# Kernel optimization log

Measured on AMD Instinct MI355X. Metric: run time of the kernel, lower is better.

## Reference

```python
import jax, jax.numpy as jnp
import numpy as np

B, Ci, H, W_ = 8, 64, 128, 128
C = 2 * Ci  # output channels of the 1x1 conv


def setup_inputs() -> dict:
    key = jax.random.key(0)
    kx, kw, kb = jax.random.split(key, 3)
    x = jax.random.normal(kx, (B, Ci, H, W_), dtype=jnp.float32)
    # Conv2d(Ci, 2*Ci, 1x1) parameters (kaiming-ish scale)
    Wc = jax.random.normal(kw, (C, Ci), dtype=jnp.float32) * (1.0 / np.float32(np.sqrt(Ci)))
    bc = jax.random.normal(kb, (C,), dtype=jnp.float32) * 0.01
    return {"x": x, "Wc": Wc, "bc": bc}


def _local_attention(y):
    # y: [B, C, H, W] conv output. 3x3 neighborhood self-attention, zero padding.
    b, c, h, w = y.shape
    yp = jnp.pad(y, ((0, 0), (0, 0), (1, 1), (1, 1)))
    # patches[:, :, k] = shifted neighborhood k (row-major 3x3, matching F.unfold order)
    patches = jnp.stack(
        [yp[:, :, di:di + h, dj:dj + w] for di in range(3) for dj in range(3)],
        axis=2,
    )  # [B, C, 9, H, W]
    mid = patches[:, :, 4]  # center pixel query, [B, C, H, W]
    scale = np.float32(1.0 / np.sqrt(c))
    scores = jnp.einsum("bcnhw,bchw->bnhw", patches, mid) * scale  # [B, 9, H, W]
    attn = jax.nn.softmax(scores, axis=1)
    out = jnp.einsum("bnhw,bcnhw->bchw", attn, patches)  # [B, C, H, W]
    return out


def reference(x, Wc, bc):
    # 1x1 conv == channel matmul
    y = jnp.einsum("bihw,oi->bohw", x, Wc) + bc[None, :, None, None]
    return _local_attention(y)
```

## Files before the change

kernel.cpp:

```cpp
#include <hip/hip_runtime.h>
#include <hip/hip_bf16.h>

typedef __attribute__((ext_vector_type(8))) short short8;
typedef __attribute__((ext_vector_type(4))) float floatx4;

#define XS_STRIDE 72
#define YS_STRIDE 128
#define OST_STRIDE 132

__device__ __forceinline__ ushort f2bf(float f) {
    union { __hip_bfloat16 h; ushort u; } cv;
    cv.h = __float2bfloat16(f);
    return cv.u;
}
__device__ __forceinline__ float bflo(unsigned int u) { return __uint_as_float(u << 16); }
__device__ __forceinline__ float bfhi(unsigned int u) { return __uint_as_float(u & 0xffff0000u); }

__device__ __forceinline__ float dot8(uint4 p, const float* cf) {
    return bflo(p.x)*cf[0] + bfhi(p.x)*cf[1] + bflo(p.y)*cf[2] + bfhi(p.y)*cf[3]
         + bflo(p.z)*cf[4] + bfhi(p.z)*cf[5] + bflo(p.w)*cf[6] + bfhi(p.w)*cf[7];
}
__device__ __forceinline__ void fma8(uint4 p, float a, float* o) {
    o[0] += a*bflo(p.x); o[1] += a*bfhi(p.x); o[2] += a*bflo(p.y); o[3] += a*bfhi(p.y);
    o[4] += a*bflo(p.z); o[5] += a*bfhi(p.z); o[6] += a*bflo(p.w); o[7] += a*bfhi(p.w);
}

__global__ __launch_bounds__(256, 2)
void attn_conv_fused(const float* __restrict__ x, const float* __restrict__ Wc,
                     const float* __restrict__ bc, float* __restrict__ out) {
    __shared__ __align__(16) unsigned char smem[81600];
    ushort* xs = (ushort*)smem;
    float*  ostage = (float*)smem;
    ushort* ys = (ushort*)(smem + 29376);

    const int tid = threadIdx.x;
    const int b  = blockIdx.z;
    const int h0 = blockIdx.y * 4;
    const int w0 = blockIdx.x * 32;
    const int lane = tid & 63;
    const int wv   = tid >> 6;

    if (tid < 204) {
        int py  = (tid * 965) >> 15;
        int pxx = tid - py * 34;
        int gh = h0 + py - 1, gw = w0 + pxx - 1;
        bool inb = (gh >= 0 && gh < 128 && gw >= 0 && gw < 128);
        ushort* dst = xs + tid * XS_STRIDE;
        if (inb) {
            const float* xp = x + (b * 64) * 16384 + gh * 128 + gw;
            #pragma unroll
            for (int c0 = 0; c0 < 64; c0 += 4) {
                float v0 = xp[(c0 + 0) << 14];
                float v1 = xp[(c0 + 1) << 14];
                float v2 = xp[(c0 + 2) << 14];
                float v3 = xp[(c0 + 3) << 14];
                unsigned int u01 = (unsigned int)f2bf(v0) | ((unsigned int)f2bf(v1) << 16);
                unsigned int u23 = (unsigned int)f2bf(v2) | ((unsigned int)f2bf(v3) << 16);
                *(uint2*)(dst + c0) = make_uint2(u01, u23);
            }
        } else {
            #pragma unroll
            for (int c0 = 0; c0 < 64; c0 += 4)
                *(uint2*)(dst + c0) = make_uint2(0u, 0u);
        }
    }

    const int col = lane & 15;
    const int kq  = lane >> 4;
    short8 bw[8][2];
    float  bias[8];
    #pragma unroll
    for (int t = 0; t < 8; ++t) {
        int c = t * 16 + col;
        bias[t] = bc[c];
        #pragma unroll
        for (int half = 0; half < 2; ++half) {
            const float* wp = Wc + c * 64 + half * 32 + kq * 8;
            float4 wa = *(const float4*)wp;
            float4 wb = *(const float4*)(wp + 4);
            short8 f;
            f[0] = (short)f2bf(wa.x); f[1] = (short)f2bf(wa.y);
            f[2] = (short)f2bf(wa.z); f[3] = (short)f2bf(wa.w);
            f[4] = (short)f2bf(wb.x); f[5] = (short)f2bf(wb.y);
            f[6] = (short)f2bf(wb.z); f[7] = (short)f2bf(wb.w);
            bw[t][half] = f;
        }
    }
    __syncthreads();

    for (int mt = wv; mt < 13; mt += 4) {
        int pxa = mt * 16 + col;
        const ushort* ap = xs + pxa * XS_STRIDE + kq * 8;
        short8 a0 = *(const short8*)(ap);
        short8 a1 = *(const short8*)(ap + 32);
        floatx4 acc[8];
        #pragma unroll
        for (int t = 0; t < 8; ++t) acc[t] = (floatx4){0.f, 0.f, 0.f, 0.f};
        #pragma unroll
        for (int t = 0; t < 8; ++t) {
            acc[t] = __builtin_amdgcn_mfma_f32_16x16x32_bf16(a0, bw[t][0], acc[t], 0, 0, 0);
            acc[t] = __builtin_amdgcn_mfma_f32_16x16x32_bf16(a1, bw[t][1], acc[t], 0, 0, 0);
        }
        #pragma unroll
        for (int r = 0; r < 4; ++r) {
            int pxr = mt * 16 + kq * 4 + r;
            if (pxr < 204) {
                int py  = (pxr * 965) >> 15;
                int pxx = pxr - py * 34;
                int gh = h0 + py - 1, gw = w0 + pxx - 1;
                bool inb = (gh >= 0 && gh < 128 && gw >= 0 && gw < 128);
                ushort* yrow = ys + pxr * YS_STRIDE + col;
                #pragma unroll
                for (int t = 0; t < 8; ++t)
                    yrow[t * 16] = f2bf(inb ? (acc[t][r] + bias[t]) : 0.f);
            }
        }
    }
    __syncthreads();

    const int g  = tid & 7;
    const int ox = tid >> 3;
    for (int oy = 0; oy < 4; ++oy) {
        int pc = (oy + 1) * 34 + (ox + 1);
        const ushort* base = ys + g * 16;
        uint4 plo[9], phi[9];
        #pragma unroll
        for (int n = 0; n < 9; ++n) {
            int pi = pc + (n / 3 - 1) * 34 + (n % 3 - 1);
            const ushort* pp = base + pi * YS_STRIDE;
            plo[n] = *(const uint4*)pp;
            phi[n] = *(const uint4*)(pp + 8);
        }
        float cf[16];
        {
            uint4 c0 = plo[4], c1 = phi[4];
            cf[0]=bflo(c0.x); cf[1]=bfhi(c0.x); cf[2]=bflo(c0.y); cf[3]=bfhi(c0.y);
            cf[4]=bflo(c0.z); cf[5]=bfhi(c0.z); cf[6]=bflo(c0.w); cf[7]=bfhi(c0.w);
            cf[8]=bflo(c1.x); cf[9]=bfhi(c1.x); cf[10]=bflo(c1.y); cf[11]=bfhi(c1.y);
            cf[12]=bflo(c1.z); cf[13]=bfhi(c1.z); cf[14]=bflo(c1.w); cf[15]=bfhi(c1.w);
        }
        float s[9];
        #pragma unroll
        for (int n = 0; n < 9; ++n)
            s[n] = dot8(plo[n], cf) + dot8(phi[n], cf + 8);
        #pragma unroll
        for (int n = 0; n < 9; ++n) {
            s[n] += __shfl_xor(s[n], 1);
            s[n] += __shfl_xor(s[n], 2);
            s[n] += __shfl_xor(s[n], 4);
            s[n] *= 0.08838834764831845f;
        }
        float m = s[0];
        #pragma unroll
        for (int n = 1; n < 9; ++n) m = fmaxf(m, s[n]);
        float e[9], sum = 0.f;
        #pragma unroll
        for (int n = 0; n < 9; ++n) { e[n] = __expf(s[n] - m); sum += e[n]; }
        float inv = 1.f / sum;

        float o[16];
        #pragma unroll
        for (int j = 0; j < 16; ++j) o[j] = 0.f;
        #pragma unroll
        for (int n = 0; n < 9; ++n) {
            float a = e[n] * inv;
            fma8(plo[n], a, o);
            fma8(phi[n], a, o + 8);
        }

        float* op = ostage + ox * OST_STRIDE + g * 16;
        #pragma unroll
        for (int k = 0; k < 4; ++k)
            *(float4*)(op + 4 * k) = make_float4(o[4*k], o[4*k+1], o[4*k+2], o[4*k+3]);
        __syncthreads();

        {
            int c = tid >> 1, half = tid & 1;
            float tmp[16];
            #pragma unroll
            for (int j = 0; j < 16; ++j)
                tmp[j] = ostage[(half * 16 + j) * OST_STRIDE + c];
            float* og = out + ((size_t)((b * 128 + c) * 128 + (h0 + oy))) * 128 + w0 + half * 16;
            #pragma unroll
            for (int k = 0; k < 4; ++k)
                *(float4*)(og + 4 * k) = make_float4(tmp[4*k], tmp[4*k+1], tmp[4*k+2], tmp[4*k+3]);
        }
        __syncthreads();
    }
}

extern "C" void kernel_launch(void* const* d_in, const int* in_sizes, int n_in,
                              void* d_out, int out_size, void* d_ws, size_t ws_size,
                              hipStream_t stream) {
    const float* x  = (const float*)d_in[0];
    const float* Wc = (const float*)d_in[1];
    const float* bc = (const float*)d_in[2];
    float* out = (float*)d_out;

    dim3 grid(4, 32, 8);
    dim3 block(256);
    attn_conv_fused<<<grid, block, 0, stream>>>(x, Wc, bc, out);
}
```

Measured before the change: 137.7 us.

## Shrink LDS footprint for three blocks per CU with swizzled conv buffer

Hoists the A-fragments into registers so the y buffer can reuse the x region. The conv output uses an XOR-swizzled unpadded layout, and the output transpose staging is split into two halves. Together these cut shared memory from about 80KB to 51KB so three blocks fit per CU. It also replaces two shuffles with DPP ops in the score reduction and remaps a flat 1D grid so consecutive blocks spread across batches. The cost is extra barriers per output row and higher register pressure from the held fragments under the tighter launch bound.

```diff
diff --git a/kernel.cpp b/kernel.cpp
--- a/kernel.cpp
+++ b/kernel.cpp
@@ -5,8 +5,6 @@
 typedef __attribute__((ext_vector_type(4))) float floatx4;
 
 #define XS_STRIDE 72
-#define YS_STRIDE 128
-#define OST_STRIDE 132
 
 __device__ __forceinline__ ushort f2bf(float f) {
     union { __hip_bfloat16 h; ushort u; } cv;
@@ -25,18 +23,24 @@
     o[4] += a*bflo(p.z); o[5] += a*bfhi(p.z); o[6] += a*bflo(p.w); o[7] += a*bfhi(p.w);
 }
 
-__global__ __launch_bounds__(256, 2)
+__device__ __forceinline__ float gsum8(float v) {
+    v += __int_as_float(__builtin_amdgcn_update_dpp(0, __float_as_int(v), 0xB1, 0xF, 0xF, false));
+    v += __int_as_float(__builtin_amdgcn_update_dpp(0, __float_as_int(v), 0x4E, 0xF, 0xF, false));
+    v += __shfl_xor(v, 4);
+    return v;
+}
+
+__global__ __launch_bounds__(256, 3)
 void attn_conv_fused(const float* __restrict__ x, const float* __restrict__ Wc,
                      const float* __restrict__ bc, float* __restrict__ out) {
-    __shared__ __align__(16) unsigned char smem[81600];
+    __shared__ __align__(16) unsigned char smem[52224];
     ushort* xs = (ushort*)smem;
-    float*  ostage = (float*)smem;
-    ushort* ys = (ushort*)(smem + 29376);
 
     const int tid = threadIdx.x;
-    const int b  = blockIdx.z;
-    const int h0 = blockIdx.y * 4;
-    const int w0 = blockIdx.x * 32;
+    const int rid = ((blockIdx.x & 7) << 7) | (blockIdx.x >> 3);
+    const int b   = rid >> 7;
+    const int h0  = ((rid >> 2) & 31) * 4;
+    const int w0  = (rid & 3) * 32;
     const int lane = tid & 63;
     const int wv   = tid >> 6;
 
@@ -88,31 +92,45 @@
     }
     __syncthreads();
 
-    for (int mt = wv; mt < 13; mt += 4) {
-        int pxa = mt * 16 + col;
-        const ushort* ap = xs + pxa * XS_STRIDE + kq * 8;
-        short8 a0 = *(const short8*)(ap);
-        short8 a1 = *(const short8*)(ap + 32);
-        floatx4 acc[8];
-        #pragma unroll
-        for (int t = 0; t < 8; ++t) acc[t] = (floatx4){0.f, 0.f, 0.f, 0.f};
-        #pragma unroll
-        for (int t = 0; t < 8; ++t) {
-            acc[t] = __builtin_amdgcn_mfma_f32_16x16x32_bf16(a0, bw[t][0], acc[t], 0, 0, 0);
-            acc[t] = __builtin_amdgcn_mfma_f32_16x16x32_bf16(a1, bw[t][1], acc[t], 0, 0, 0);
-        }
-        #pragma unroll
-        for (int r = 0; r < 4; ++r) {
-            int pxr = mt * 16 + kq * 4 + r;
-            if (pxr < 204) {
-                int py  = (pxr * 965) >> 15;
-                int pxx = pxr - py * 34;
-                int gh = h0 + py - 1, gw = w0 + pxx - 1;
-                bool inb = (gh >= 0 && gh < 128 && gw >= 0 && gw < 128);
-                ushort* yrow = ys + pxr * YS_STRIDE + col;
-                #pragma unroll
-                for (int t = 0; t < 8; ++t)
-                    yrow[t * 16] = f2bf(inb ? (acc[t][r] + bias[t]) : 0.f);
+    short8 af0[4], af1[4];
+    #pragma unroll
+    for (int i = 0; i < 4; ++i) {
+        int mt = wv + i * 4;
+        if (mt < 13) {
+            const ushort* ap = xs + (mt * 16 + col) * XS_STRIDE + kq * 8;
+            af0[i] = *(const short8*)(ap);
+            af1[i] = *(const short8*)(ap + 32);
+        }
+    }
+    __syncthreads();
+
+    #pragma unroll
+    for (int i = 0; i < 4; ++i) {
+        int mt = wv + i * 4;
+        if (mt < 13) {
+            floatx4 acc[8];
+            #pragma unroll
+            for (int t = 0; t < 8; ++t) acc[t] = (floatx4){0.f, 0.f, 0.f, 0.f};
+            #pragma unroll
+            for (int t = 0; t < 8; ++t) {
+                acc[t] = __builtin_amdgcn_mfma_f32_16x16x32_bf16(af0[i], bw[t][0], acc[t], 0, 0, 0);
+                acc[t] = __builtin_amdgcn_mfma_f32_16x16x32_bf16(af1[i], bw[t][1], acc[t], 0, 0, 0);
+            }
+            #pragma unroll
+            for (int r = 0; r < 4; ++r) {
+                int pxr = mt * 16 + kq * 4 + r;
+                if (pxr < 204) {
+                    int py  = (pxr * 965) >> 15;
+                    int pxx = pxr - py * 34;
+                    int gh = h0 + py - 1, gw = w0 + pxx - 1;
+                    bool inb = (gh >= 0 && gh < 128 && gw >= 0 && gw < 128);
+                    char* yrow = (char*)smem + pxr * 256;
+                    int swz = (pxr & 7) << 5;
+                    #pragma unroll
+                    for (int t = 0; t < 8; ++t)
+                        *(ushort*)(yrow + (((t * 32) ^ swz) + col * 2)) =
+                            f2bf(inb ? (acc[t][r] + bias[t]) : 0.f);
+                }
             }
         }
     }
@@ -122,14 +140,13 @@
     const int ox = tid >> 3;
     for (int oy = 0; oy < 4; ++oy) {
         int pc = (oy + 1) * 34 + (ox + 1);
-        const ushort* base = ys + g * 16;
         uint4 plo[9], phi[9];
         #pragma unroll
         for (int n = 0; n < 9; ++n) {
             int pi = pc + (n / 3 - 1) * 34 + (n % 3 - 1);
-            const ushort* pp = base + pi * YS_STRIDE;
+            const char* pp = (const char*)smem + pi * 256 + ((g * 32) ^ ((pi & 7) << 5));
             plo[n] = *(const uint4*)pp;
-            phi[n] = *(const uint4*)(pp + 8);
+            phi[n] = *(const uint4*)(pp + 16);
         }
         float cf[16];
         {
@@ -144,12 +161,8 @@
         for (int n = 0; n < 9; ++n)
             s[n] = dot8(plo[n], cf) + dot8(phi[n], cf + 8);
         #pragma unroll
-        for (int n = 0; n < 9; ++n) {
-            s[n] += __shfl_xor(s[n], 1);
-            s[n] += __shfl_xor(s[n], 2);
-            s[n] += __shfl_xor(s[n], 4);
-            s[n] *= 0.08838834764831845f;
-        }
+        for (int n = 0; n < 9; ++n)
+            s[n] = gsum8(s[n]) * 0.08838834764831845f;
         float m = s[0];
         #pragma unroll
         for (int n = 1; n < 9; ++n) m = fmaxf(m, s[n]);
@@ -168,24 +181,41 @@
             fma8(phi[n], a, o + 8);
         }
 
-        float* op = ostage + ox * OST_STRIDE + g * 16;
-        #pragma unroll
-        for (int k = 0; k < 4; ++k)
-            *(float4*)(op + 4 * k) = make_float4(o[4*k], o[4*k+1], o[4*k+2], o[4*k+3]);
-        __syncthreads();
-
+        float* ost = (float*)((char*)smem + oy * 8704);
+        __syncthreads();
+        if (ox < 16) {
+            float* op = ost + ox * 132 + g * 16;
+            #pragma unroll
+            for (int k = 0; k < 4; ++k)
+                *(float4*)(op + 4 * k) = make_float4(o[4*k], o[4*k+1], o[4*k+2], o[4*k+3]);
+        }
+        __syncthreads();
         {
-            int c = tid >> 1, half = tid & 1;
-            float tmp[16];
-            #pragma unroll
-            for (int j = 0; j < 16; ++j)
-                tmp[j] = ostage[(half * 16 + j) * OST_STRIDE + c];
-            float* og = out + ((size_t)((b * 128 + c) * 128 + (h0 + oy))) * 128 + w0 + half * 16;
+            int c = tid >> 1, q = tid & 1;
+            float tmp[8];
+            #pragma unroll
+            for (int j = 0; j < 8; ++j) tmp[j] = ost[(q * 8 + j) * 132 + c];
+            float* og = out + ((size_t)((b * 128 + c) * 128 + (h0 + oy))) * 128 + w0 + q * 8;
+            *(float4*)og       = make_float4(tmp[0], tmp[1], tmp[2], tmp[3]);
+            *(float4*)(og + 4) = make_float4(tmp[4], tmp[5], tmp[6], tmp[7]);
+        }
+        __syncthreads();
+        if (ox >= 16) {
+            float* op = ost + (ox - 16) * 132 + g * 16;
             #pragma unroll
             for (int k = 0; k < 4; ++k)
-                *(float4*)(og + 4 * k) = make_float4(tmp[4*k], tmp[4*k+1], tmp[4*k+2], tmp[4*k+3]);
-        }
-        __syncthreads();
+                *(float4*)(op + 4 * k) = make_float4(o[4*k], o[4*k+1], o[4*k+2], o[4*k+3]);
+        }
+        __syncthreads();
+        {
+            int c = tid >> 1, q = tid & 1;
+            float tmp[8];
+            #pragma unroll
+            for (int j = 0; j < 8; ++j) tmp[j] = ost[(q * 8 + j) * 132 + c];
+            float* og = out + ((size_t)((b * 128 + c) * 128 + (h0 + oy))) * 128 + w0 + 16 + q * 8;
+            *(float4*)og       = make_float4(tmp[0], tmp[1], tmp[2], tmp[3]);
+            *(float4*)(og + 4) = make_float4(tmp[4], tmp[5], tmp[6], tmp[7]);
+        }
     }
 }
 
@@ -197,7 +227,7 @@
     const float* bc = (const float*)d_in[2];
     float* out = (float*)d_out;
 
-    dim3 grid(4, 32, 8);
+    dim3 grid(1024);
     dim3 block(256);
     attn_conv_fused<<<grid, block, 0, stream>>>(x, Wc, bc, out);
 }
```

New measurement: 164.5 us. 19.4% more time.

## Swizzle shared-memory layouts, use DPP reductions, and remap block order

Applied to the files above, without the earlier changes.

The conv output tile moves from a flat stride-128 layout to two XOR-swizzled half-planes, one for channels 0-7 and one for 8-15 within each 16-channel group, to cut LDS bank conflicts on both the MFMA writeback and the neighborhood loads. The output staging buffer also uses an XOR swizzle in place of padding. The first two steps of the 8-lane score reduction use DPP instead of ds_swizzle shuffles. The grid becomes 1-D with a remapped block index so consecutive blocks spread across batches, which may change L2 and XCD locality. The extra address arithmetic could offset part of the benefit.

```diff
diff --git a/kernel.cpp b/kernel.cpp
--- a/kernel.cpp
+++ b/kernel.cpp
@@ -5,8 +5,8 @@
 typedef __attribute__((ext_vector_type(4))) float floatx4;
 
 #define XS_STRIDE 72
-#define YS_STRIDE 128
-#define OST_STRIDE 132
+#define PBASE 29376
+#define QBASE 55504
 
 __device__ __forceinline__ ushort f2bf(float f) {
     union { __hip_bfloat16 h; ushort u; } cv;
@@ -25,18 +25,25 @@
     o[4] += a*bflo(p.z); o[5] += a*bfhi(p.z); o[6] += a*bflo(p.w); o[7] += a*bfhi(p.w);
 }
 
+__device__ __forceinline__ float gsum8(float v) {
+    v += __int_as_float(__builtin_amdgcn_update_dpp(0, __float_as_int(v), 0xB1, 0xF, 0xF, false));
+    v += __int_as_float(__builtin_amdgcn_update_dpp(0, __float_as_int(v), 0x4E, 0xF, 0xF, false));
+    v += __shfl_xor(v, 4);
+    return v;
+}
+
 __global__ __launch_bounds__(256, 2)
 void attn_conv_fused(const float* __restrict__ x, const float* __restrict__ Wc,
                      const float* __restrict__ bc, float* __restrict__ out) {
-    __shared__ __align__(16) unsigned char smem[81600];
+    __shared__ __align__(16) unsigned char smem[81632];
     ushort* xs = (ushort*)smem;
-    float*  ostage = (float*)smem;
-    ushort* ys = (ushort*)(smem + 29376);
+    char* smc = (char*)smem;
 
     const int tid = threadIdx.x;
-    const int b  = blockIdx.z;
-    const int h0 = blockIdx.y * 4;
-    const int w0 = blockIdx.x * 32;
+    const int rid = ((blockIdx.x & 7) << 7) | (blockIdx.x >> 3);
+    const int b   = rid >> 7;
+    const int h0  = ((rid >> 2) & 31) * 4;
+    const int w0  = (rid & 3) * 32;
     const int lane = tid & 63;
     const int wv   = tid >> 6;
 
@@ -88,6 +95,8 @@
     }
     __syncthreads();
 
+    char* wbase = smc + (col < 8 ? PBASE : QBASE);
+    const int cb2 = (col & 7) * 2;
     for (int mt = wv; mt < 13; mt += 4) {
         int pxa = mt * 16 + col;
         const ushort* ap = xs + pxa * XS_STRIDE + kq * 8;
@@ -109,10 +118,12 @@
                 int pxx = pxr - py * 34;
                 int gh = h0 + py - 1, gw = w0 + pxx - 1;
                 bool inb = (gh >= 0 && gh < 128 && gw >= 0 && gw < 128);
-                ushort* yrow = ys + pxr * YS_STRIDE + col;
+                char* prow = wbase + pxr * 128;
+                int swz = (pxr & 7) << 4;
                 #pragma unroll
                 for (int t = 0; t < 8; ++t)
-                    yrow[t * 16] = f2bf(inb ? (acc[t][r] + bias[t]) : 0.f);
+                    *(ushort*)(prow + (((t * 16) ^ swz) + cb2)) =
+                        f2bf(inb ? (acc[t][r] + bias[t]) : 0.f);
             }
         }
     }
@@ -122,14 +133,13 @@
     const int ox = tid >> 3;
     for (int oy = 0; oy < 4; ++oy) {
         int pc = (oy + 1) * 34 + (ox + 1);
-        const ushort* base = ys + g * 16;
         uint4 plo[9], phi[9];
         #pragma unroll
         for (int n = 0; n < 9; ++n) {
             int pi = pc + (n / 3 - 1) * 34 + (n % 3 - 1);
-            const ushort* pp = base + pi * YS_STRIDE;
+            const char* pp = smc + PBASE + pi * 128 + ((g * 16) ^ ((pi & 7) << 4));
             plo[n] = *(const uint4*)pp;
-            phi[n] = *(const uint4*)(pp + 8);
+            phi[n] = *(const uint4*)(pp + (QBASE - PBASE));
         }
         float cf[16];
         {
@@ -144,12 +154,8 @@
         for (int n = 0; n < 9; ++n)
             s[n] = dot8(plo[n], cf) + dot8(phi[n], cf + 8);
         #pragma unroll
-        for (int n = 0; n < 9; ++n) {
-            s[n] += __shfl_xor(s[n], 1);
-            s[n] += __shfl_xor(s[n], 2);
-            s[n] += __shfl_xor(s[n], 4);
-            s[n] *= 0.08838834764831845f;
-        }
+        for (int n = 0; n < 9; ++n)
+            s[n] = gsum8(s[n]) * 0.08838834764831845f;
         float m = s[0];
         #pragma unroll
         for (int n = 1; n < 9; ++n) m = fmaxf(m, s[n]);
@@ -168,18 +174,25 @@
             fma8(phi[n], a, o + 8);
         }
 
-        float* op = ostage + ox * OST_STRIDE + g * 16;
-        #pragma unroll
-        for (int k = 0; k < 4; ++k)
-            *(float4*)(op + 4 * k) = make_float4(o[4*k], o[4*k+1], o[4*k+2], o[4*k+3]);
+        {
+            char* orow = smc + ox * 512;
+            int xsw = ox & 7;
+            #pragma unroll
+            for (int k = 0; k < 4; ++k)
+                *(float4*)(orow + (((g * 4 + k) ^ xsw) << 4)) =
+                    make_float4(o[4*k], o[4*k+1], o[4*k+2], o[4*k+3]);
+        }
         __syncthreads();
 
         {
             int c = tid >> 1, half = tid & 1;
+            int lc = c >> 2, fo = (c & 3) << 2;
             float tmp[16];
             #pragma unroll
-            for (int j = 0; j < 16; ++j)
-                tmp[j] = ostage[(half * 16 + j) * OST_STRIDE + c];
+            for (int j = 0; j < 16; ++j) {
+                int row = half * 16 + j;
+                tmp[j] = *(const float*)(smc + row * 512 + ((lc ^ (row & 7)) << 4) + fo);
+            }
             float* og = out + ((size_t)((b * 128 + c) * 128 + (h0 + oy))) * 128 + w0 + half * 16;
             #pragma unroll
             for (int k = 0; k < 4; ++k)
@@ -197,7 +210,7 @@
     const float* bc = (const float*)d_in[2];
     float* out = (float*)d_out;
 
-    dim3 grid(4, 32, 8);
+    dim3 grid(1024);
     dim3 block(256);
     attn_conv_fused<<<grid, block, 0, stream>>>(x, Wc, bc, out);
 }
```

Measured after the change: 130.9 us. 5.0% less time.
